# Kernel tuning notes

Hardware: AMD Instinct MI355X
Metric: run time of the kernel (lower is better)

Reference implementation:

```python
import jax, jax.numpy as jnp
import numpy as np

N_NODES = 100000
N_EDGES = 3200000
F = 32          # n_node_features
L = 50          # n_node_labels
EL = 10         # n_edge_labels
K = 16          # out_dim (graph_data.num_classes)


def setup_inputs() -> dict:
    key = jax.random.key(0)
    ks = jax.random.split(key, 12)
    x = jax.random.normal(ks[0], (N_NODES, F), dtype=jnp.float32)
    node_labels = jax.random.randint(ks[1], (N_NODES,), 0, L, dtype=jnp.int32)
    edge_src = jax.random.randint(ks[2], (N_EDGES,), 0, N_NODES, dtype=jnp.int32)
    edge_dst = jax.random.randint(ks[3], (N_EDGES,), 0, N_NODES, dtype=jnp.int32)
    edge_labels = jax.random.randint(ks[4], (N_EDGES,), 0, EL, dtype=jnp.int32)
    s = 0.1
    W1 = jax.random.normal(ks[5], (L, L, EL), dtype=jnp.float32) * s
    b1 = jax.random.normal(ks[6], (L,), dtype=jnp.float32) * s
    W2 = jax.random.normal(ks[7], (L, L, EL), dtype=jnp.float32) * s
    b2 = jax.random.normal(ks[8], (L,), dtype=jnp.float32) * s
    W3 = jax.random.normal(ks[9], (L, L, EL), dtype=jnp.float32) * s
    b3 = jax.random.normal(ks[10], (L,), dtype=jnp.float32) * s
    kr1, kr2 = jax.random.split(ks[11])
    Wr = jax.random.normal(kr1, (L, F, K), dtype=jnp.float32) * s
    br = jax.random.normal(kr2, (K,), dtype=jnp.float32) * s
    return {"x": x, "W1": W1, "b1": b1, "W2": W2, "b2": b2, "W3": W3, "b3": b3,
            "Wr": Wr, "br": br, "node_labels": node_labels,
            "edge_src": edge_src, "edge_dst": edge_dst, "edge_labels": edge_labels}


def _conv(x, W, b, node_labels, edge_src, edge_dst, edge_labels):
    # weight_rule_wf: per-edge scalar weight indexed by (src label, dst label, edge label)
    w_e = W[node_labels[edge_src], node_labels[edge_dst], edge_labels]  # [E]
    msgs = w_e[:, None] * x[edge_src]                                   # [E, F]
    agg = jax.ops.segment_sum(msgs, edge_dst, num_segments=x.shape[0])  # [N, F]
    # node_label_rule bias: per-node bias indexed by node label, then Tanh
    return jnp.tanh(agg + b[node_labels][:, None])


def reference(x, W1, b1, W2, b2, W3, b3, Wr, br,
              node_labels, edge_src, edge_dst, edge_labels):
    h = _conv(x, W1, b1, node_labels, edge_src, edge_dst, edge_labels)
    h = _conv(h, W2, b2, node_labels, edge_src, edge_dst, edge_labels)
    h = _conv(h, W3, b3, node_labels, edge_src, edge_dst, edge_labels)
    # GraphResizeLayer (node_label_rule): out[k] = sum_i Wr[label_i, f, k] * h[i, f] + br[k]
    # equivalent efficient form: pre-aggregate node features by label, then contract.
    sums = jax.ops.segment_sum(h, node_labels, num_segments=Wr.shape[0])  # [L, F]
    out = jnp.tanh(jnp.einsum('lf,lfk->k', sums, Wr) + br)                # [K]
    return out
```

## Files before the change

### kernel.cpp

```cpp
#include <hip/hip_runtime.h>
#include <hip/hip_bf16.h>
#include <hip/hip_fp8.h>

#define NN 100000
#define NE 3200000
#define FF 32
#define LL 50
#define ELB 10
#define KK 16

#define CH 4096
#define NBLK_P1 782
#define NBUK 391
#define CAP 9216

typedef float floatx2 __attribute__((ext_vector_type(2)));

__device__ __forceinline__ float fast_tanh(float x) {
    float e = __expf(2.0f * x);
    return 1.0f - 2.0f / (e + 1.0f);
}

__global__ __launch_bounds__(512) void p1_scatter(const int* __restrict__ esrc,
                                                  const int* __restrict__ edst,
                                                  const int* __restrict__ elab,
                                                  const float* __restrict__ x,
                                                  unsigned* __restrict__ xb,
                                                  int* __restrict__ cursor,
                                                  unsigned* __restrict__ recs) {
    __shared__ int lcnt[NBUK];
    __shared__ int lbase[NBUK];
    __shared__ int sdst[CH];
    int tid = threadIdx.x;
    for (int i = blockIdx.x * 512 + tid; i < NN * FF / 4; i += NBLK_P1 * 512) {
        float4 v = ((const float4*)x)[i];
        __hip_fp8_e4m3 a(v.x), b(v.y), c(v.z), d(v.w);
        xb[i] = (unsigned)a.__x | ((unsigned)b.__x << 8) |
                ((unsigned)c.__x << 16) | ((unsigned)d.__x << 24);
    }
    for (int i = tid; i < NBUK; i += 512) lcnt[i] = 0;
    __syncthreads();
    long e0 = (long)blockIdx.x * CH;
    long rem = NE - e0;
    int cnt = rem < CH ? (int)rem : CH;
    int nq = cnt >> 2;
    const int4* edst4 = (const int4*)(edst + e0);
    const int4* esrc4 = (const int4*)(esrc + e0);
    const int4* elab4 = (const int4*)(elab + e0);
    for (int i = tid; i < nq; i += 512) {
        int4 d = edst4[i];
        ((int4*)sdst)[i] = d;
        atomicAdd(&lcnt[d.x >> 8], 1);
        atomicAdd(&lcnt[d.y >> 8], 1);
        atomicAdd(&lcnt[d.z >> 8], 1);
        atomicAdd(&lcnt[d.w >> 8], 1);
    }
    __syncthreads();
    for (int i = tid; i < NBUK; i += 512) {
        int c = lcnt[i];
        lbase[i] = c ? atomicAdd(&cursor[i], c) : 0;
        lcnt[i] = 0;
    }
    __syncthreads();
    for (int i = tid; i < nq; i += 512) {
        int4 s4 = esrc4[i];
        int4 l4 = elab4[i];
        int4 d4 = ((const int4*)sdst)[i];
#pragma unroll
        for (int k = 0; k < 4; ++k) {
            int s  = (&s4.x)[k];
            int d  = (&d4.x)[k];
            int el = (&l4.x)[k];
            int b = d >> 8;
            int ofs = atomicAdd(&lcnt[b], 1);
            int rel = lbase[b] + ofs;
            if (rel < CAP)
                recs[b * CAP + rel] =
                    ((unsigned)s << 12) | ((unsigned)el << 8) | (unsigned)(d & 255);
        }
    }
}

__global__ __launch_bounds__(512) void p2_local(const int* __restrict__ cursor,
                                                const unsigned* __restrict__ recs,
                                                const int* __restrict__ labels,
                                                unsigned* __restrict__ packed,
                                                int* __restrict__ gstart,
                                                int* __restrict__ gcnt) {
    __shared__ int deg[256], loff[256], lcur[256], sc[256], labd[256];
    int b = blockIdx.x, tid = threadIdx.x;
    int base = b * CAP;
    int n = cursor[b];
    if (n > CAP) n = CAP;
    if (tid < 256) {
        int node = (b << 8) + tid;
        deg[tid] = 0;
        lcur[tid] = 0;
        labd[tid] = (node < NN) ? labels[node] : 0;
    }
    __syncthreads();
    for (int i = tid; i < n; i += 512)
        atomicAdd(&deg[(int)(recs[base + i] & 255)], 1);
    __syncthreads();
    if (tid < 256) sc[tid] = deg[tid];
    __syncthreads();
    for (int ofs = 1; ofs < 256; ofs <<= 1) {
        int t = (tid >= ofs && tid < 256) ? sc[tid - ofs] : 0;
        __syncthreads();
        if (tid < 256) sc[tid] += t;
        __syncthreads();
    }
    if (tid < 256) {
        loff[tid] = sc[tid] - deg[tid];
        int node = (b << 8) + tid;
        if (node < NN) { gstart[node] = base + loff[tid]; gcnt[node] = deg[tid]; }
    }
    __syncthreads();
    for (int i = tid; i < n; i += 512) {
        unsigned r = recs[base + i];
        int dl  = (int)(r & 255);
        int el  = (int)((r >> 8) & 15);
        int src = (int)(r >> 12);
        int widx = labels[src] * (LL * ELB) + labd[dl] * ELB + el;
        int ofs = atomicAdd(&lcur[dl], 1);
        packed[base + loff[dl] + ofs] = ((unsigned)widx << 17) | (unsigned)src;
    }
}

__global__ __launch_bounds__(256) void conv_kernel(const unsigned char* __restrict__ xin,
                                                   unsigned char* __restrict__ hout,
                                                   const int* __restrict__ gstart,
                                                   const int* __restrict__ gcnt,
                                                   const unsigned* __restrict__ packed,
                                                   const float* __restrict__ Wtab,
                                                   const float* __restrict__ bias,
                                                   const int* __restrict__ labels) {
    __shared__ unsigned stage[8][64];
    int tid = threadIdx.x;
    int hw = tid >> 5, lane = tid & 31;
    int node = (blockIdx.x << 3) + hw;
    int s = gstart[node];
    int n = gcnt[node];
    int eg = lane >> 3;
    int fg = (lane & 7) << 2;
    float4 acc = {0.f, 0.f, 0.f, 0.f};
    for (int base = 0; base < n; base += 32) {
        float w = 0.f;
        unsigned so = 0u;
        int idx = base + lane;
        if (idx < n) {
            unsigned p = packed[s + idx];
            w = Wtab[p >> 17];
            so = (p & 0x1FFFFu) << 5;
        }
        ((uint2*)&stage[hw][0])[lane] = make_uint2(__float_as_uint(w), so);
        __builtin_amdgcn_wave_barrier();
#pragma unroll
        for (int j = 0; j < 8; ++j) {
            uint2 ws = ((const uint2*)&stage[hw][0])[j * 4 + eg];
            unsigned pv = *(const unsigned*)(xin + ws.y + fg);
            floatx2 lo = __builtin_amdgcn_cvt_pk_f32_fp8((int)pv, false);
            floatx2 hi = __builtin_amdgcn_cvt_pk_f32_fp8((int)pv, true);
            float we = __uint_as_float(ws.x);
            acc.x += we * lo.x;
            acc.y += we * lo.y;
            acc.z += we * hi.x;
            acc.w += we * hi.y;
        }
        __builtin_amdgcn_wave_barrier();
    }
    acc.x += __shfl_xor(acc.x, 8);  acc.y += __shfl_xor(acc.y, 8);
    acc.z += __shfl_xor(acc.z, 8);  acc.w += __shfl_xor(acc.w, 8);
    acc.x += __shfl_xor(acc.x, 16); acc.y += __shfl_xor(acc.y, 16);
    acc.z += __shfl_xor(acc.z, 16); acc.w += __shfl_xor(acc.w, 16);
    if (lane < 8) {
        float bb = bias[labels[node]];
        __hip_fp8_e4m3 q0(fast_tanh(acc.x + bb));
        __hip_fp8_e4m3 q1(fast_tanh(acc.y + bb));
        __hip_fp8_e4m3 q2(fast_tanh(acc.z + bb));
        __hip_fp8_e4m3 q3(fast_tanh(acc.w + bb));
        unsigned pk = (unsigned)q0.__x | ((unsigned)q1.__x << 8) |
                      ((unsigned)q2.__x << 16) | ((unsigned)q3.__x << 24);
        ((unsigned*)(hout + ((long)node << 5)))[lane] = pk;
    }
}

__global__ __launch_bounds__(256) void lsum_kernel(const unsigned* __restrict__ h,
                                                   const int* __restrict__ labels,
                                                   float* __restrict__ sums) {
    __shared__ float ls[LL * FF];
    int tid = threadIdx.x;
    for (int i = tid; i < LL * FF; i += 256) ls[i] = 0.f;
    __syncthreads();
    for (int i = blockIdx.x * 256 + tid; i < NN * 8; i += gridDim.x * 256) {
        unsigned pv = h[i];
        int nodei = i >> 3;
        int fb = (i & 7) << 2;
        int l = labels[nodei];
        floatx2 lo = __builtin_amdgcn_cvt_pk_f32_fp8((int)pv, false);
        floatx2 hi = __builtin_amdgcn_cvt_pk_f32_fp8((int)pv, true);
        float* bp = &ls[l * FF + fb];
        atomicAdd(bp + 0, lo.x);
        atomicAdd(bp + 1, lo.y);
        atomicAdd(bp + 2, hi.x);
        atomicAdd(bp + 3, hi.y);
    }
    __syncthreads();
    for (int i = tid; i < LL * FF; i += 256) atomicAdd(&sums[i], ls[i]);
}

__global__ __launch_bounds__(256) void resize_kernel(const float* __restrict__ sums,
                                                     const float* __restrict__ Wr,
                                                     const float* __restrict__ br,
                                                     float* __restrict__ out) {
    __shared__ float red[256][KK];
    int tid = threadIdx.x;
    float acc[KK];
#pragma unroll
    for (int k = 0; k < KK; ++k) acc[k] = 0.f;
    for (int p = tid; p < LL * FF; p += 256) {
        float sv = sums[p];
#pragma unroll
        for (int k = 0; k < KK; ++k) acc[k] += sv * Wr[p * KK + k];
    }
#pragma unroll
    for (int k = 0; k < KK; ++k) red[tid][k] = acc[k];
    __syncthreads();
    for (int sft = 128; sft > 0; sft >>= 1) {
        if (tid < sft) {
#pragma unroll
            for (int k = 0; k < KK; ++k) red[tid][k] += red[tid + sft][k];
        }
        __syncthreads();
    }
    if (tid < KK) out[tid] = fast_tanh(red[0][tid] + br[tid]);
}

extern "C" void kernel_launch(void* const* d_in, const int* in_sizes, int n_in,
                              void* d_out, int out_size, void* d_ws, size_t ws_size,
                              hipStream_t stream) {
    const float* x   = (const float*)d_in[0];
    const float* W1  = (const float*)d_in[1];
    const float* b1  = (const float*)d_in[2];
    const float* W2  = (const float*)d_in[3];
    const float* b2  = (const float*)d_in[4];
    const float* W3  = (const float*)d_in[5];
    const float* b3  = (const float*)d_in[6];
    const float* Wr  = (const float*)d_in[7];
    const float* br  = (const float*)d_in[8];
    const int* labels = (const int*)d_in[9];
    const int* esrc   = (const int*)d_in[10];
    const int* edst   = (const int*)d_in[11];
    const int* elab   = (const int*)d_in[12];
    float* out = (float*)d_out;

    char* ws = (char*)d_ws;
    size_t o = 0;
    auto alloc = [&](size_t bytes) -> void* {
        void* p = ws + o;
        o += (bytes + 255) & ~(size_t)255;
        return p;
    };
    char* regionA = (char*)alloc((size_t)NBUK * CAP * sizeof(unsigned));
    unsigned* recs = (unsigned*)regionA;
    unsigned char* h1 = (unsigned char*)regionA;
    unsigned char* h2 = (unsigned char*)(regionA + (size_t)NN * FF);

    unsigned* packed = (unsigned*)alloc((size_t)NBUK * CAP * sizeof(unsigned));
    unsigned* xb     = (unsigned*)alloc((size_t)NN * FF);
    int* cursor = (int*)alloc(NBUK * sizeof(int));
    float* sums = (float*)alloc(LL * FF * sizeof(float));
    int* gstart = (int*)alloc(NN * sizeof(int));
    int* gcnt   = (int*)alloc(NN * sizeof(int));

    size_t msz = (size_t)((char*)sums - (char*)cursor) + LL * FF * sizeof(float);
    hipMemsetAsync(cursor, 0, msz, stream);

    p1_scatter<<<NBLK_P1, 512, 0, stream>>>(esrc, edst, elab, x, xb, cursor, recs);
    p2_local<<<NBUK, 512, 0, stream>>>(cursor, recs, labels, packed, gstart, gcnt);

    conv_kernel<<<NN / 8, 256, 0, stream>>>((const unsigned char*)xb, h1, gstart, gcnt, packed, W1, b1, labels);
    conv_kernel<<<NN / 8, 256, 0, stream>>>(h1, h2, gstart, gcnt, packed, W2, b2, labels);
    conv_kernel<<<NN / 8, 256, 0, stream>>>(h2, h1, gstart, gcnt, packed, W3, b3, labels);

    lsum_kernel<<<256, 256, 0, stream>>>((const unsigned*)h1, labels, sums);
    resize_kernel<<<1, 256, 0, stream>>>(sums, Wr, br, out);
}
```

Baseline: 316.3 us.

## Stage bucketed edge records in LDS and write them out coalesced

The scatter pass now handles 8192 edges per block with half as many blocks. A block-wide prefix scan over bucket counts lays records out sorted by bucket in shared memory, and a final loop writes them to global memory so neighbouring threads hit neighbouring addresses instead of scattering single writes. This trades extra LDS traffic (about 72KB per block), a scan with many barriers, and re-reading edst from global for fewer, better-coalesced global writes. Fewer blocks also means less parallelism for the fp8 conversion of x and the edge pass.

```diff
diff --git a/kernel.cpp b/kernel.cpp
--- a/kernel.cpp
+++ b/kernel.cpp
@@ -9,8 +9,8 @@
 #define ELB 10
 #define KK 16
 
-#define CH 4096
-#define NBLK_P1 782
+#define CH 8192
+#define NBLK_P1 391
 #define NBUK 391
 #define CAP 9216
 
@@ -29,8 +29,11 @@
                                                   int* __restrict__ cursor,
                                                   unsigned* __restrict__ recs) {
     __shared__ int lcnt[NBUK];
+    __shared__ int lofs[NBUK];
     __shared__ int lbase[NBUK];
-    __shared__ int sdst[CH];
+    __shared__ int sc[512];
+    __shared__ unsigned srec[CH];
+    __shared__ unsigned sgad[CH];
     int tid = threadIdx.x;
     for (int i = blockIdx.x * 512 + tid; i < NN * FF / 4; i += NBLK_P1 * 512) {
         float4 v = ((const float4*)x)[i];
@@ -49,35 +52,49 @@
     const int4* elab4 = (const int4*)(elab + e0);
     for (int i = tid; i < nq; i += 512) {
         int4 d = edst4[i];
-        ((int4*)sdst)[i] = d;
         atomicAdd(&lcnt[d.x >> 8], 1);
         atomicAdd(&lcnt[d.y >> 8], 1);
         atomicAdd(&lcnt[d.z >> 8], 1);
         atomicAdd(&lcnt[d.w >> 8], 1);
     }
     __syncthreads();
-    for (int i = tid; i < NBUK; i += 512) {
-        int c = lcnt[i];
-        lbase[i] = c ? atomicAdd(&cursor[i], c) : 0;
-        lcnt[i] = 0;
+    sc[tid] = (tid < NBUK) ? lcnt[tid] : 0;
+    __syncthreads();
+    for (int ofs = 1; ofs < 512; ofs <<= 1) {
+        int t = (tid >= ofs) ? sc[tid - ofs] : 0;
+        __syncthreads();
+        sc[tid] += t;
+        __syncthreads();
+    }
+    if (tid < NBUK) {
+        int c = lcnt[tid];
+        lofs[tid] = sc[tid] - c;
+        lbase[tid] = c ? atomicAdd(&cursor[tid], c) : 0;
+        lcnt[tid] = 0;
     }
     __syncthreads();
     for (int i = tid; i < nq; i += 512) {
         int4 s4 = esrc4[i];
         int4 l4 = elab4[i];
-        int4 d4 = ((const int4*)sdst)[i];
+        int4 d4 = edst4[i];
 #pragma unroll
         for (int k = 0; k < 4; ++k) {
             int s  = (&s4.x)[k];
             int d  = (&d4.x)[k];
             int el = (&l4.x)[k];
             int b = d >> 8;
-            int ofs = atomicAdd(&lcnt[b], 1);
-            int rel = lbase[b] + ofs;
-            if (rel < CAP)
-                recs[b * CAP + rel] =
-                    ((unsigned)s << 12) | ((unsigned)el << 8) | (unsigned)(d & 255);
+            int pos = atomicAdd(&lcnt[b], 1);
+            int slot = lofs[b] + pos;
+            srec[slot] = ((unsigned)s << 12) | ((unsigned)el << 8) | (unsigned)(d & 255);
+            int rel = lbase[b] + pos;
+            sgad[slot] = (rel < CAP) ? (unsigned)(b * CAP + rel) : 0xFFFFFFFFu;
         }
+    }
+    __syncthreads();
+    for (int i = tid; i < cnt; i += 512) {
+        unsigned g = sgad[i];
+        if (g != 0xFFFFFFFFu)
+            recs[g] = srec[i];
     }
 }
 
```

Result: faster. 292.2 us (-7.6%).
